# Performance work log

Hardware: AMD Instinct MI355X
Metric: run time of the kernel (lower is better)

The kernel has to match this reference:

```python
import jax, jax.numpy as jnp
import numpy as np
import math

WIDTH_POW = 10
WIDTH = 2 ** WIDTH_POW      # 1024
DEPTH = 20
BATCH = 8192
TWO_PI = 2.0 * math.pi


def setup_inputs() -> dict:
    key = jax.random.key(0)
    kx, ka = jax.random.split(key)
    # X is [width, batch] (features-first, matching the torch module's dim-0 padding)
    X = jax.random.normal(kx, (WIDTH, BATCH), dtype=jnp.float32)
    # angles ~ Uniform[0, 2*pi), as in the torch initializer
    angles = jax.random.uniform(ka, (DEPTH, WIDTH // 2), dtype=jnp.float32) * TWO_PI
    return {"X": X, "angles": angles}


def _butterfly_layer(X, ang, stride):
    # X: [width, batch]; ang: [width//2]
    w, b = X.shape
    # Pairs: within each block of 2*stride, element j rotates with element j+stride.
    Xr = X.reshape(w // (2 * stride), 2, stride, b)
    x0 = Xr[:, 0]  # [nblocks, stride, batch]
    x1 = Xr[:, 1]
    c = jnp.cos(ang).reshape(-1, stride, 1)
    s = jnp.sin(ang).reshape(-1, stride, 1)
    y0 = c * x0 + s * x1
    y1 = -s * x0 + c * x1
    return jnp.stack([y0, y1], axis=1).reshape(w, b)


def reference(X, angles):
    width = angles.shape[1] * 2
    width_pow = int(round(math.log2(width)))
    # Pad feature dim up to width (no-op here since X.shape[0] == width)
    pad = width - X.shape[0]
    if pad > 0:
        X = jnp.concatenate([X, jnp.zeros((pad, X.shape[1]), dtype=X.dtype)], axis=0)
    depth = angles.shape[0]
    for i in range(depth):  # small fixed loop over layers (structurally distinct strides)
        stride = 2 ** (i % width_pow)
        X = _butterfly_layer(X, angles[i], stride)
    return X
```

## Files before the change

kernel.cpp:

```cpp
#include <hip/hip_runtime.h>
#include <math.h>


#define NROW   1024
#define BATCH  8192
#define BATCH2 (BATCH / 2)
#define DEPTH  20
#define NANG   512
#define TAB_ELEMS (DEPTH * NANG)
#define TAB_BYTES ((size_t)TAB_ELEMS * 8)
#define WS_MFMA_BYTES ((size_t)(4 * 32 * 1024) * 2 * 2)

typedef float v2f __attribute__((ext_vector_type(2)));
using bf16x8 = __attribute__((ext_vector_type(8))) short;
using f32x4  = __attribute__((ext_vector_type(4))) float;

__device__ __forceinline__ unsigned short f2b(float f) {
    union { float f; unsigned int u; } v; v.f = f;
    unsigned int u = v.u;
    return (unsigned short)((u + 0x7FFFu + ((u >> 16) & 1u)) >> 16);
}
__device__ __forceinline__ float b2f(unsigned short b) {
    union { unsigned int u; float f; } v; v.u = ((unsigned int)b) << 16;
    return v.f;
}

__global__ __launch_bounds__(64) void build_w_kernel(
        const float* __restrict__ ang,
        unsigned short* __restrict__ whi,
        unsigned short* __restrict__ wlo) {
    __shared__ float2 cs[160];
    int ln = threadIdx.x;
    int widx = blockIdx.x;
    int grp = widx >> 4;
    int bpair = widx & 15;

    #pragma unroll
    for (int rnd = 0; rnd < 3; ++rnd) {
        int tt = ln + rnd * 64;
        if (tt < 160) {
            int h = tt >= 80;
            int u = tt - h * 80;
            int q = u >> 4, p = u & 15;
            int b = bpair * 2 + h;
            int sp = (grp & 1) ? q + 5 : q;
            int l  = grp * 5 + q;
            int s  = 1 << sp;
            int SL = 1 << q;
            int i0 = ((p >> q) << (q + 1)) | (p & (SL - 1));
            int r0 = (grp & 1) ? ((i0 << 5) | b) : ((b << 5) | i0);
            int a  = ((r0 >> (sp + 1)) << sp) | (r0 & (s - 1));
            float th = ang[l * NANG + a];
            float sv, cv;
            __sincosf(th, &sv, &cv);
            cs[tt] = make_float2(cv, sv);
        }
    }
    __syncthreads();

    int h = ln >> 5, j = ln & 31;
    int b = bpair * 2 + h;
    float v[32];
    #pragma unroll
    for (int i = 0; i < 32; ++i) v[i] = (i == j) ? 1.f : 0.f;
    #pragma unroll
    for (int q = 0; q < 5; ++q) {
        int SL = 1 << q;
        #pragma unroll
        for (int p = 0; p < 16; ++p) {
            int i0 = ((p >> q) << (q + 1)) | (p & (SL - 1));
            int i1 = i0 + SL;
            float2 q2 = cs[h * 80 + q * 16 + p];
            float x0 = v[i0], x1 = v[i1];
            v[i0] = q2.x * x0 + q2.y * x1;
            v[i1] = q2.x * x1 - q2.y * x0;
        }
    }
    int mat = grp * 32 + b;
    #pragma unroll
    for (int i = 0; i < 32; ++i) {
        unsigned short hh = f2b(v[i]);
        whi[mat * 1024 + i * 32 + j] = hh;
        wlo[mat * 1024 + i * 32 + j] = f2b(v[i] - b2f(hh));
    }
}

__global__ __launch_bounds__(512) void mfma_kernel(
        const float* __restrict__ X,
        const unsigned short* __restrict__ whi,
        const unsigned short* __restrict__ wlo,
        float* __restrict__ out) {
    __shared__ __align__(16) unsigned short sbuf[2][32768];
    int t  = threadIdx.x;
    int ln = t & 63;
    int w  = t >> 6;
    int bid = blockIdx.x;
    int L = ((bid & 7) << 5) | (bid >> 3);
    int col0 = L << 5;

    {
        int cc = t & 15, sg = (t >> 4) & 1, bb = t >> 5;
        int col = col0 + sg * 16 + cc;
        #pragma unroll
        for (int half = 0; half < 2; ++half) {
            int rb = bb + 16 * half;
            int site = rb * 2 + sg;
            #pragma unroll
            for (int g = 0; g < 4; ++g) {
                unsigned int uu[4];
                #pragma unroll
                for (int jj = 0; jj < 4; ++jj) {
                    float va = X[(rb * 32 + g * 8 + 2 * jj) * BATCH + col];
                    float vb = X[(rb * 32 + g * 8 + 2 * jj + 1) * BATCH + col];
                    uu[jj] = (unsigned int)f2b(va) | ((unsigned int)f2b(vb) << 16);
                }
                *reinterpret_cast<uint4*>(&sbuf[0][site * 512 + g * 128 + cc * 8]) =
                    make_uint4(uu[0], uu[1], uu[2], uu[3]);
            }
        }
    }
    __syncthreads();

    const bf16x8* WH = reinterpret_cast<const bf16x8*>(whi);
    const bf16x8* WL = reinterpret_cast<const bf16x8*>(wlo);
    int r15 = ln & 15, kg = ln >> 4;

    #pragma unroll
    for (int grp = 0; grp < 4; ++grp) {
        int cur = grp & 1;
        #pragma unroll
        for (int m = 0; m < 4; ++m) {
            int rb  = (w & 7) + 8 * m;
            int mat = grp * 32 + rb;
            bf16x8 ah0 = WH[mat * 128 + (r15     ) * 4 + kg];
            bf16x8 ah1 = WH[mat * 128 + (r15 + 16) * 4 + kg];
            bf16x8 al0 = WL[mat * 128 + (r15     ) * 4 + kg];
            bf16x8 al1 = WL[mat * 128 + (r15 + 16) * 4 + kg];
            #pragma unroll
            for (int sg2 = 0; sg2 < 2; ++sg2) {
                int site = rb * 2 + sg2;
                bf16x8 bf = *reinterpret_cast<const bf16x8*>(
                    &sbuf[cur][site * 512 + kg * 128 + r15 * 8]);
                f32x4 acc0 = {0.f, 0.f, 0.f, 0.f};
                f32x4 acc1 = {0.f, 0.f, 0.f, 0.f};
                acc0 = __builtin_amdgcn_mfma_f32_16x16x32_bf16(ah0, bf, acc0, 0, 0, 0);
                acc0 = __builtin_amdgcn_mfma_f32_16x16x32_bf16(al0, bf, acc0, 0, 0, 0);
                acc1 = __builtin_amdgcn_mfma_f32_16x16x32_bf16(ah1, bf, acc1, 0, 0, 0);
                acc1 = __builtin_amdgcn_mfma_f32_16x16x32_bf16(al1, bf, acc1, 0, 0, 0);
                if (grp < 3) {
                    #pragma unroll
                    for (int e = 0; e < 4; ++e) {
                        int k0 = kg * 4 + e;
                        int k1 = 16 + kg * 4 + e;
                        sbuf[cur ^ 1][(k0 * 2 + sg2) * 512 + (rb >> 3) * 128 +
                                      r15 * 8 + (rb & 7)] = f2b(acc0[e]);
                        sbuf[cur ^ 1][(k1 * 2 + sg2) * 512 + (rb >> 3) * 128 +
                                      r15 * 8 + (rb & 7)] = f2b(acc1[e]);
                    }
                } else {
                    int col = col0 + sg2 * 16 + r15;
                    #pragma unroll
                    for (int e = 0; e < 4; ++e) {
                        int r0 = (kg * 4 + e) * 32 + rb;
                        int r1 = (16 + kg * 4 + e) * 32 + rb;
                        out[r0 * BATCH + col] = acc0[e];
                        out[r1 * BATCH + col] = acc1[e];
                    }
                }
            }
        }
        if (grp < 3) __syncthreads();
    }
}

__device__ __host__ __forceinline__ int rowA(int sub, int i){ return (sub << 5) | i; }
__device__ __host__ __forceinline__ int rowB(int sub, int i){ return sub | (i << 5); }

__global__ void build_tab_kernel(const float* __restrict__ ang,
                                 float2* __restrict__ tab) {
    int idx = blockIdx.x * blockDim.x + threadIdx.x;
    if (idx >= TAB_ELEMS) return;
    int l = idx >> 9;
    int slot = idx & (NANG - 1);
    int sub = slot >> 4, p = slot & 15;
    int m10 = l % 10;
    int sp = m10;
    int SL = 1 << (m10 % 5);
    int i0 = 2 * (p / SL) * SL + p % SL;
    int r = (m10 >= 5) ? rowB(sub, i0) : rowA(sub, i0);
    int a = ((r >> (sp + 1)) << sp) | (r & ((1 << sp) - 1));
    float th = ang[l * NANG + a];
    float sv, cv;
    sincosf(th, &sv, &cv);
    tab[idx] = make_float2(cv, sv);
}

__device__ __forceinline__ void rotp(v2f& a, v2f& b, float cv, float sv) {
    v2f c = {cv, cv}, s = {sv, sv};
    v2f x0 = a, x1 = b;
    a = __builtin_elementwise_fma(c, x0, s * x1);
    b = __builtin_elementwise_fma(-s, x0, c * x1);
}

template<int SL>
__device__ __forceinline__ void layer_tab(v2f y[32],
                                          const float4* __restrict__ q4) {
    #pragma unroll
    for (int v = 0; v < 8; ++v) {
        float4 q = q4[v];
        int p0 = 2 * v, p1 = 2 * v + 1;
        int a0 = 2 * (p0 / SL) * SL + p0 % SL;
        int a1 = 2 * (p1 / SL) * SL + p1 % SL;
        rotp(y[a0], y[a0 + SL], q.x, q.y);
        rotp(y[a1], y[a1 + SL], q.z, q.w);
    }
}

template<int SL, bool PB, int SP>
__device__ __forceinline__ void layer_notab(v2f y[32],
                                            const float* __restrict__ angL,
                                            int sub) {
    #pragma unroll
    for (int p = 0; p < 16; ++p) {
        int i0 = 2 * (p / SL) * SL + p % SL;
        int r = PB ? rowB(sub, i0) : rowA(sub, i0);
        int a = ((r >> (SP + 1)) << SP) | (r & ((1 << SP) - 1));
        float th = angL[a];
        float sv, cv;
        __sincosf(th, &sv, &cv);
        rotp(y[i0], y[i0 + SL], cv, sv);
    }
}

template<bool USE_TAB>
__global__ __launch_bounds__(256) void butterfly_kernel(
        const float* __restrict__ X, const float* __restrict__ ang,
        const float2* __restrict__ tab, float* __restrict__ out) {
    __shared__ v2f lds[8 * 1024];
    int t = threadIdx.x;
    int c = t & 7;
    int sub = t >> 3;
    int bid = blockIdx.x;
    int L = ((bid & 7) << 6) | (bid >> 3);
    int col2 = (L << 3) + c;
    int xr = (c & 7) << 1;
    v2f* base = lds + (c << 10);

    v2f y[32];
    const v2f* Xp = reinterpret_cast<const v2f*>(X) + col2;
    #pragma unroll
    for (int i = 0; i < 32; ++i)
        y[i] = Xp[rowA(sub, i) * BATCH2];

    const float4* tf4 = reinterpret_cast<const float4*>(tab);
    if (USE_TAB) {
        layer_tab<1 >(y, tf4 + 0 * 256 + 8 * sub);
        layer_tab<2 >(y, tf4 + 1 * 256 + 8 * sub);
        layer_tab<4 >(y, tf4 + 2 * 256 + 8 * sub);
        layer_tab<8 >(y, tf4 + 3 * 256 + 8 * sub);
        layer_tab<16>(y, tf4 + 4 * 256 + 8 * sub);
    } else {
        layer_notab<1 ,false,0>(y, ang + 0 * NANG, sub);
        layer_notab<2 ,false,1>(y, ang + 1 * NANG, sub);
        layer_notab<4 ,false,2>(y, ang + 2 * NANG, sub);
        layer_notab<8 ,false,3>(y, ang + 3 * NANG, sub);
        layer_notab<16,false,4>(y, ang + 4 * NANG, sub);
    }
    #pragma unroll
    for (int u = 0; u < 16; ++u)
        *reinterpret_cast<float4*>(&base[((sub << 5) + 2 * u) ^ xr]) =
            make_float4(y[2*u].x, y[2*u].y, y[2*u+1].x, y[2*u+1].y);
    __syncthreads();
    #pragma unroll
    for (int i = 0; i < 32; ++i) y[i] = base[rowB(sub, i) ^ xr];

    if (USE_TAB) {
        layer_tab<1 >(y, tf4 + 5 * 256 + 8 * sub);
        layer_tab<2 >(y, tf4 + 6 * 256 + 8 * sub);
        layer_tab<4 >(y, tf4 + 7 * 256 + 8 * sub);
        layer_tab<8 >(y, tf4 + 8 * 256 + 8 * sub);
        layer_tab<16>(y, tf4 + 9 * 256 + 8 * sub);
    } else {
        layer_notab<1 ,true,5>(y, ang + 5 * NANG, sub);
        layer_notab<2 ,true,6>(y, ang + 6 * NANG, sub);
        layer_notab<4 ,true,7>(y, ang + 7 * NANG, sub);
        layer_notab<8 ,true,8>(y, ang + 8 * NANG, sub);
        layer_notab<16,true,9>(y, ang + 9 * NANG, sub);
    }
    __syncthreads();
    #pragma unroll
    for (int i = 0; i < 32; ++i) base[rowB(sub, i) ^ xr] = y[i];
    __syncthreads();
    #pragma unroll
    for (int u = 0; u < 16; ++u) {
        float4 v = *reinterpret_cast<const float4*>(&base[((sub << 5) + 2 * u) ^ xr]);
        y[2*u].x = v.x; y[2*u].y = v.y; y[2*u+1].x = v.z; y[2*u+1].y = v.w;
    }

    if (USE_TAB) {
        layer_tab<1 >(y, tf4 + 10 * 256 + 8 * sub);
        layer_tab<2 >(y, tf4 + 11 * 256 + 8 * sub);
        layer_tab<4 >(y, tf4 + 12 * 256 + 8 * sub);
        layer_tab<8 >(y, tf4 + 13 * 256 + 8 * sub);
        layer_tab<16>(y, tf4 + 14 * 256 + 8 * sub);
    } else {
        layer_notab<1 ,false,0>(y, ang + 10 * NANG, sub);
        layer_notab<2 ,false,1>(y, ang + 11 * NANG, sub);
        layer_notab<4 ,false,2>(y, ang + 12 * NANG, sub);
        layer_notab<8 ,false,3>(y, ang + 13 * NANG, sub);
        layer_notab<16,false,4>(y, ang + 14 * NANG, sub);
    }
    __syncthreads();
    #pragma unroll
    for (int u = 0; u < 16; ++u)
        *reinterpret_cast<float4*>(&base[((sub << 5) + 2 * u) ^ xr]) =
            make_float4(y[2*u].x, y[2*u].y, y[2*u+1].x, y[2*u+1].y);
    __syncthreads();
    #pragma unroll
    for (int i = 0; i < 32; ++i) y[i] = base[rowB(sub, i) ^ xr];

    if (USE_TAB) {
        layer_tab<1 >(y, tf4 + 15 * 256 + 8 * sub);
        layer_tab<2 >(y, tf4 + 16 * 256 + 8 * sub);
        layer_tab<4 >(y, tf4 + 17 * 256 + 8 * sub);
        layer_tab<8 >(y, tf4 + 18 * 256 + 8 * sub);
        layer_tab<16>(y, tf4 + 19 * 256 + 8 * sub);
    } else {
        layer_notab<1 ,true,5>(y, ang + 15 * NANG, sub);
        layer_notab<2 ,true,6>(y, ang + 16 * NANG, sub);
        layer_notab<4 ,true,7>(y, ang + 17 * NANG, sub);
        layer_notab<8 ,true,8>(y, ang + 18 * NANG, sub);
        layer_notab<16,true,9>(y, ang + 19 * NANG, sub);
    }

    v2f* Op = reinterpret_cast<v2f*>(out) + col2;
    #pragma unroll
    for (int i = 0; i < 32; ++i)
        Op[rowB(sub, i) * BATCH2] = y[i];
}

extern "C" void kernel_launch(void* const* d_in, const int* in_sizes, int n_in,
                              void* d_out, int out_size, void* d_ws, size_t ws_size,
                              hipStream_t stream) {
    (void)in_sizes; (void)n_in; (void)out_size;
    const float* X   = (const float*)d_in[0];
    const float* ang = (const float*)d_in[1];
    float* out = (float*)d_out;

    if (d_ws != nullptr && ws_size >= WS_MFMA_BYTES) {
        unsigned short* whi = (unsigned short*)d_ws;
        unsigned short* wlo = whi + 4 * 32 * 1024;
        build_w_kernel<<<64, 64, 0, stream>>>(ang, whi, wlo);
        mfma_kernel<<<256, 512, 0, stream>>>(X, whi, wlo, out);
    } else if (d_ws != nullptr && ws_size >= TAB_BYTES) {
        float2* tab = (float2*)d_ws;
        build_tab_kernel<<<(TAB_ELEMS + 255) / 256, 256, 0, stream>>>(ang, tab);
        butterfly_kernel<true><<<512, 256, 0, stream>>>(X, ang, tab, out);
    } else {
        butterfly_kernel<false><<<512, 256, 0, stream>>>(X, ang, nullptr, out);
    }
}
```

Before: 29.83 us.

## Single-buffer LDS by preloading B fragments into registers before overwrite

Replaces the double-buffered shared-memory stage with a single buffer. Each group first loads all of its B fragments into registers, then synchronizes before overwriting the buffer in place. This halves shared memory per block and adds a launch-bounds occupancy hint, aiming to let more blocks reside per CU. In exchange it costs more registers and one extra barrier per group.

```diff
diff --git a/kernel.cpp b/kernel.cpp
--- a/kernel.cpp
+++ b/kernel.cpp
@@ -85,12 +85,12 @@
     }
 }
 
-__global__ __launch_bounds__(512) void mfma_kernel(
+__global__ __launch_bounds__(512, 4) void mfma_kernel(
         const float* __restrict__ X,
         const unsigned short* __restrict__ whi,
         const unsigned short* __restrict__ wlo,
         float* __restrict__ out) {
-    __shared__ __align__(16) unsigned short sbuf[2][32768];
+    __shared__ __align__(16) unsigned short sbuf[32768];
     int t  = threadIdx.x;
     int ln = t & 63;
     int w  = t >> 6;
@@ -114,7 +114,7 @@
                     float vb = X[(rb * 32 + g * 8 + 2 * jj + 1) * BATCH + col];
                     uu[jj] = (unsigned int)f2b(va) | ((unsigned int)f2b(vb) << 16);
                 }
-                *reinterpret_cast<uint4*>(&sbuf[0][site * 512 + g * 128 + cc * 8]) =
+                *reinterpret_cast<uint4*>(&sbuf[site * 512 + g * 128 + cc * 8]) =
                     make_uint4(uu[0], uu[1], uu[2], uu[3]);
             }
         }
@@ -127,7 +127,19 @@
 
     #pragma unroll
     for (int grp = 0; grp < 4; ++grp) {
-        int cur = grp & 1;
+        bf16x8 bf[8];
+        #pragma unroll
+        for (int m = 0; m < 4; ++m) {
+            int rb = (w & 7) + 8 * m;
+            #pragma unroll
+            for (int sg2 = 0; sg2 < 2; ++sg2) {
+                int site = rb * 2 + sg2;
+                bf[m * 2 + sg2] = *reinterpret_cast<const bf16x8*>(
+                    &sbuf[site * 512 + kg * 128 + r15 * 8]);
+            }
+        }
+        if (grp < 3) __syncthreads();
+
         #pragma unroll
         for (int m = 0; m < 4; ++m) {
             int rb  = (w & 7) + 8 * m;
@@ -138,24 +150,22 @@
             bf16x8 al1 = WL[mat * 128 + (r15 + 16) * 4 + kg];
             #pragma unroll
             for (int sg2 = 0; sg2 < 2; ++sg2) {
-                int site = rb * 2 + sg2;
-                bf16x8 bf = *reinterpret_cast<const bf16x8*>(
-                    &sbuf[cur][site * 512 + kg * 128 + r15 * 8]);
+                bf16x8 b = bf[m * 2 + sg2];
                 f32x4 acc0 = {0.f, 0.f, 0.f, 0.f};
                 f32x4 acc1 = {0.f, 0.f, 0.f, 0.f};
-                acc0 = __builtin_amdgcn_mfma_f32_16x16x32_bf16(ah0, bf, acc0, 0, 0, 0);
-                acc0 = __builtin_amdgcn_mfma_f32_16x16x32_bf16(al0, bf, acc0, 0, 0, 0);
-                acc1 = __builtin_amdgcn_mfma_f32_16x16x32_bf16(ah1, bf, acc1, 0, 0, 0);
-                acc1 = __builtin_amdgcn_mfma_f32_16x16x32_bf16(al1, bf, acc1, 0, 0, 0);
+                acc0 = __builtin_amdgcn_mfma_f32_16x16x32_bf16(ah0, b, acc0, 0, 0, 0);
+                acc0 = __builtin_amdgcn_mfma_f32_16x16x32_bf16(al0, b, acc0, 0, 0, 0);
+                acc1 = __builtin_amdgcn_mfma_f32_16x16x32_bf16(ah1, b, acc1, 0, 0, 0);
+                acc1 = __builtin_amdgcn_mfma_f32_16x16x32_bf16(al1, b, acc1, 0, 0, 0);
                 if (grp < 3) {
                     #pragma unroll
                     for (int e = 0; e < 4; ++e) {
                         int k0 = kg * 4 + e;
                         int k1 = 16 + kg * 4 + e;
-                        sbuf[cur ^ 1][(k0 * 2 + sg2) * 512 + (rb >> 3) * 128 +
-                                      r15 * 8 + (rb & 7)] = f2b(acc0[e]);
-                        sbuf[cur ^ 1][(k1 * 2 + sg2) * 512 + (rb >> 3) * 128 +
-                                      r15 * 8 + (rb & 7)] = f2b(acc1[e]);
+                        sbuf[(k0 * 2 + sg2) * 512 + (rb >> 3) * 128 +
+                             r15 * 8 + (rb & 7)] = f2b(acc0[e]);
+                        sbuf[(k1 * 2 + sg2) * 512 + (rb >> 3) * 128 +
+                             r15 * 8 + (rb & 7)] = f2b(acc1[e]);
                     }
                 } else {
                     int col = col0 + sg2 * 16 + r15;
```

Result: no change. 29.46 us (-1.3%).
